# Kernel optimization log

Measured on AMD Instinct MI355X. Metric: run time of the kernel, lower is better.

## Reference

```python
import jax, jax.numpy as jnp
import numpy as np

RHO = 0.1

def setup_inputs() -> dict:
    key = jax.random.key(0)
    k1, k2 = jax.random.split(key)
    B, C, H, W = 64, 256, 56, 56
    features = jax.random.normal(k1, (B, C, H, W), dtype=jnp.float32)
    grad = jax.random.normal(k2, (B, C, H, W), dtype=jnp.float32)
    return {"features": features, "grad": grad}


def reference(features, grad):
    # attribution = relu(grad * features), elementwise
    attribution = jax.nn.relu(grad * features)
    B = attribution.shape[0]
    flat_attr = attribution.reshape(B, -1)          # [B, C*H*W]
    k = int(RHO * flat_attr.shape[1])               # static: 80281
    topk_val, _ = jax.lax.top_k(flat_attr, k)       # [B, k], descending
    threshold = topk_val[:, -1].reshape(-1, 1, 1, 1)  # k-th largest per sample
    mask = (attribution <= threshold).astype(features.dtype)
    return features * mask
```

## Files before the change

### kernel.cpp

```cpp
#include <hip/hip_runtime.h>

namespace {
constexpr int NS   = 64;
constexpr int NPS  = 802816;
constexpr int NPSV = NPS / 4;
constexpr unsigned KSEL = 80281u;
constexpr unsigned SENT = 0xFFFFFFFFu;
constexpr int NB   = 8192;
constexpr int GX   = 32;
constexpr int SEGV = NPSV / GX;
constexpr int SEG  = NPS / GX;
constexpr int PAIRCAP = 1024;
constexpr int CAP_LDS = 20480;
constexpr int BRB  = 8;
constexpr int CHUNKS = 128;
constexpr int CH_STRIDE = NPSV / CHUNKS;
constexpr unsigned RU_RANK = 12129u;
constexpr unsigned RL_RANK = 14086u;
constexpr int GXA  = 64;
constexpr int SEGCAP2 = 20736;
constexpr int TAILF4  = 1056;
typedef float f32x4 __attribute__((ext_vector_type(4)));
}

__device__ __forceinline__ void nt_store4(float4* dst, const float4& v) {
    f32x4 w; w.x = v.x; w.y = v.y; w.z = v.z; w.w = v.w;
    __builtin_nontemporal_store(w, reinterpret_cast<f32x4*>(dst));
}

template <int NBINS>
__device__ void select_in_lds(const unsigned* __restrict__ h, unsigned K,
                              unsigned* bin, unsigned* rem) {
    constexpr int BPT = NBINS / 256;
    __shared__ unsigned cs[256];
    __shared__ unsigned fB, fR;
    const int t = threadIdx.x;
    unsigned s = 0;
    for (int j = 0; j < BPT; ++j) s += h[t * BPT + j];
    cs[t] = s;
    if (t == 0) { fB = SENT; fR = 0u; }
    __syncthreads();
    unsigned suf = 0;
    for (int j = t + 1; j < 256; ++j) suf += cs[j];
    if (suf < K && suf + s >= K) {
        unsigned cur = suf;
        for (int j = BPT - 1; j >= 0; --j) {
            const unsigned c = h[t * BPT + j];
            if (cur < K && cur + c >= K) { fB = (unsigned)(t * BPT + j); fR = K - cur; break; }
            cur += c;
        }
    }
    __syncthreads();
    const unsigned rb = fB, rr = fR;
    __syncthreads();
    *bin = rb; *rem = rr;
}

__global__ __launch_bounds__(256) void bracket_kernel(const float4* __restrict__ f,
                                                      const float4* __restrict__ g,
                                                      unsigned short* __restrict__ bh,
                                                      unsigned* __restrict__ fail) {
    __shared__ unsigned h[NB];
    const int jb = blockIdx.x, b = blockIdx.y, t = threadIdx.x;
    if (jb == 0 && b == 0 && t == 0) fail[0] = 0u;
    for (int k = t; k < NB; k += 256) h[k] = 0u;
    __syncthreads();
    const size_t base = (size_t)b * NPSV;
#define HBIN(p) { if ((p) > 0.0f) atomicAdd(&h[__float_as_uint(p) >> 18], 1u); }
    for (int c = 0; c < CHUNKS / BRB; c += 2) {
        const int ch = jb * (CHUNKS / BRB) + c;
        const size_t i0 = base + (size_t)ch * CH_STRIDE + t;
        const size_t i1 = base + (size_t)(ch + 1) * CH_STRIDE + t;
        const float4 fa = f[i0], fb = f[i1];
        const float4 ga = g[i0], gb = g[i1];
        HBIN(fa.x * ga.x) HBIN(fa.y * ga.y) HBIN(fa.z * ga.z) HBIN(fa.w * ga.w)
        HBIN(fb.x * gb.x) HBIN(fb.y * gb.y) HBIN(fb.z * gb.z) HBIN(fb.w * gb.w)
    }
#undef HBIN
    __syncthreads();
    unsigned short* o = bh + (size_t)(b * BRB + jb) * NB;
    for (int k = t; k < NB; k += 256) o[k] = (unsigned short)h[k];
}

__global__ __launch_bounds__(256) void bracket_scan_kernel(const unsigned short* __restrict__ bh,
                                                           unsigned* __restrict__ binLU) {
    __shared__ unsigned h[NB];
    const int b = blockIdx.x, t = threadIdx.x;
    for (int k = t; k < NB; k += 256) {
        unsigned s = 0;
        const unsigned short* p = bh + (size_t)b * BRB * NB + k;
        for (int j = 0; j < BRB; ++j) s += p[(size_t)j * NB];
        h[k] = s;
    }
    __syncthreads();
    unsigned bU, rU, bL, rL;
    select_in_lds<NB>(h, RU_RANK, &bU, &rU);
    select_in_lds<NB>(h, RL_RANK, &bL, &rL);
    if (t == 0) {
        binLU[2 * b]     = (bL == SENT) ? 0u : bL;
        binLU[2 * b + 1] = (bU == SENT) ? (unsigned)(NB - 1) : bU;
    }
}

__global__ __launch_bounds__(256) void scatter0_kernel(const float4* __restrict__ f,
                                                       const float4* __restrict__ g,
                                                       float4* __restrict__ out,
                                                       unsigned* __restrict__ pv,
                                                       unsigned* __restrict__ ppos,
                                                       const unsigned* __restrict__ binLU,
                                                       unsigned* __restrict__ cnts,
                                                       unsigned* __restrict__ chis,
                                                       unsigned* __restrict__ fail) {
    const int j = blockIdx.x, b = blockIdx.y, t = threadIdx.x;
    const unsigned binL = binLU[2 * b], binU = binLU[2 * b + 1];
    __shared__ unsigned cnt;
    __shared__ unsigned wsum[4];
    if (t == 0) cnt = 0u;
    __syncthreads();
    const size_t segp = (size_t)(b * GX + j) * PAIRCAP;
    const size_t base = (size_t)b * NPSV + (size_t)j * SEGV;
    unsigned chi = 0;
#define PROC(FC, PC, I4, CIDX, OC) { \
        const float p_ = (FC) * (PC); \
        const unsigned u_ = __float_as_uint(p_); \
        const unsigned pre_ = u_ >> 18; \
        const bool pos_ = p_ > 0.0f; \
        const bool drop_ = pos_ && (pre_ > binU); \
        OC = drop_ ? 0.0f : (FC); \
        chi += drop_; \
        if (pos_ && pre_ >= binL && pre_ <= binU) { \
            const unsigned x_ = atomicAdd(&cnt, 1u); \
            if (x_ < PAIRCAP) { pv[segp + x_] = u_; ppos[segp + x_] = (unsigned)((j * SEGV + (I4)) * 4) + CIDX; } \
        } }
#define PROC4(FV, GV, I4, OV) \
        PROC(FV.x, GV.x, I4, 0u, OV.x) PROC(FV.y, GV.y, I4, 1u, OV.y) \
        PROC(FV.z, GV.z, I4, 2u, OV.z) PROC(FV.w, GV.w, I4, 3u, OV.w)

    constexpr int FULL = SEGV / 1024;
    for (int it = 0; it < FULL; ++it) {
        const int i0 = it * 1024 + t;
        const float4 f0 = f[base + i0];
        const float4 f1 = f[base + i0 + 256];
        const float4 f2 = f[base + i0 + 512];
        const float4 f3 = f[base + i0 + 768];
        const float4 g0 = g[base + i0];
        const float4 g1 = g[base + i0 + 256];
        const float4 g2 = g[base + i0 + 512];
        const float4 g3 = g[base + i0 + 768];
        float4 o0, o1, o2, o3;
        PROC4(f0, g0, i0,       o0)
        PROC4(f1, g1, i0 + 256, o1)
        PROC4(f2, g2, i0 + 512, o2)
        PROC4(f3, g3, i0 + 768, o3)
        nt_store4(&out[base + i0],       o0);
        nt_store4(&out[base + i0 + 256], o1);
        nt_store4(&out[base + i0 + 512], o2);
        nt_store4(&out[base + i0 + 768], o3);
    }
    {
        const int i = FULL * 1024 + t;
        if (i < SEGV) {
            const float4 fv = f[base + i];
            const float4 gv = g[base + i];
            float4 o;
            PROC4(fv, gv, i, o)
            nt_store4(&out[base + i], o);
        }
    }
#undef PROC4
#undef PROC
    for (int off = 32; off; off >>= 1) chi += __shfl_down(chi, off);
    if ((t & 63) == 0) wsum[t >> 6] = chi;
    __syncthreads();
    if (t == 0) {
        chis[b * GX + j] = wsum[0] + wsum[1] + wsum[2] + wsum[3];
        const unsigned c = cnt;
        cnts[b * GX + j] = c;
        if (c > PAIRCAP) fail[0] = 1u;
    }
}

__global__ __launch_bounds__(256) void select0_kernel(const unsigned* __restrict__ pv,
                                                      const unsigned* __restrict__ binLU,
                                                      const unsigned* __restrict__ cnts,
                                                      const unsigned* __restrict__ chis,
                                                      unsigned* __restrict__ fail,
                                                      float* __restrict__ thrF) {
    if (fail[0]) return;
    const int b = blockIdx.x, t = threadIdx.x;
    __shared__ unsigned vals[CAP_LDS];
    __shared__ unsigned hist[NB];
    __shared__ unsigned soff[GX + 1];
    __shared__ unsigned sh_chi;
    if (t == 0) {
        unsigned o = 0;
        for (int j = 0; j < GX; ++j) { soff[j] = o; o += cnts[b * GX + j]; }
        soff[GX] = o;
        unsigned c = 0;
        for (int j = 0; j < GX; ++j) c += chis[b * GX + j];
        sh_chi = c;
    }
    __syncthreads();
    const unsigned ncand = soff[GX];
    const unsigned chi = sh_chi;
    if (chi >= KSEL) { if (t == 0) fail[0] = 1u; return; }
    const unsigned Krem = KSEL - chi;
    if (Krem > ncand) {
        if (binLU[2 * b] == 0u) { if (t == 0) thrF[b] = 0.0f; }
        else                    { if (t == 0) fail[0] = 1u; }
        return;
    }
    if (ncand > CAP_LDS) { if (t == 0) fail[0] = 1u; return; }
    for (int j = 0; j < GX; ++j) {
        const unsigned c = soff[j + 1] - soff[j];
        const unsigned* s = pv + (size_t)(b * GX + j) * PAIRCAP;
        for (unsigned i = t; i < c; i += 256) vals[soff[j] + i] = s[i];
    }
    for (int k = t; k < NB; k += 256) hist[k] = 0u;
    __syncthreads();
    for (unsigned i = t; i < ncand; i += 256) atomicAdd(&hist[vals[i] >> 18], 1u);
    __syncthreads();
    unsigned P1, r1; select_in_lds<NB>(hist, Krem, &P1, &r1);
    __syncthreads();
    for (int k = t; k < NB; k += 256) hist[k] = 0u;
    __syncthreads();
    for (unsigned i = t; i < ncand; i += 256) {
        const unsigned u = vals[i];
        if ((u >> 18) == P1) atomicAdd(&hist[(u >> 5) & (NB - 1u)], 1u);
    }
    __syncthreads();
    unsigned P2, r2; select_in_lds<NB>(hist, r1, &P2, &r2);
    __syncthreads();
    if (t < 32) hist[t] = 0u;
    __syncthreads();
    const unsigned pref = (P1 << 13) | P2;
    for (unsigned i = t; i < ncand; i += 256) {
        const unsigned u = vals[i];
        if ((u >> 5) == pref) atomicAdd(&hist[u & 31u], 1u);
    }
    __syncthreads();
    if (t == 0) {
        unsigned cur = 0, b3 = 0;
        for (int q = 31; q >= 0; --q) {
            const unsigned c = hist[q];
            if (cur < r2 && cur + c >= r2) { b3 = (unsigned)q; break; }
            cur += c;
        }
        thrF[b] = __uint_as_float((P1 << 18) | (P2 << 5) | b3);
    }
}

__global__ __launch_bounds__(256) void fixup0_kernel(const unsigned* __restrict__ pv,
                                                     const unsigned* __restrict__ ppos,
                                                     const unsigned* __restrict__ cnts,
                                                     const unsigned* __restrict__ fail,
                                                     const float* __restrict__ thrF,
                                                     float* __restrict__ out) {
    if (fail[0]) return;
    const int j = blockIdx.x, b = blockIdx.y, t = threadIdx.x;
    const float thr = thrF[b];
    const unsigned c = cnts[b * GX + j];
    const unsigned* v = pv + (size_t)(b * GX + j) * PAIRCAP;
    const unsigned* q = ppos + (size_t)(b * GX + j) * PAIRCAP;
    float* o = out + (size_t)b * NPS;
    for (unsigned i = t; i < c; i += 256) {
        if (__uint_as_float(v[i]) > thr) o[q[i]] = 0.0f;
    }
}

__global__ __launch_bounds__(256) void scatter_fb_kernel(const float4* __restrict__ f,
                                                         const float4* __restrict__ g,
                                                         unsigned* __restrict__ list,
                                                         unsigned* __restrict__ cnts,
                                                         unsigned* __restrict__ chis,
                                                         const unsigned* __restrict__ fail,
                                                         int mode, int segCap) {
    if (mode == 1 && fail[0] == 0u) return;
    const int j = blockIdx.x, b = blockIdx.y, t = threadIdx.x;
    __shared__ unsigned cnt;
    if (t == 0) cnt = 0u;
    __syncthreads();
    unsigned* __restrict__ seg = list + (size_t)b * NPS + (size_t)j * SEG;
    const size_t base = (size_t)b * NPSV + (size_t)j * SEGV;
    for (int i = t; i < SEGV; i += 256) {
        const float4 fv = f[base + i];
        const float4 gv = g[base + i];
        const float p0 = fv.x * gv.x, p1 = fv.y * gv.y, p2 = fv.z * gv.z, p3 = fv.w * gv.w;
#define PROCF(p) { if ((p) > 0.0f) { const unsigned x = atomicAdd(&cnt, 1u); \
                   if ((int)x < segCap) seg[x] = __float_as_uint(p); } }
        PROCF(p0) PROCF(p1) PROCF(p2) PROCF(p3)
#undef PROCF
    }
    __syncthreads();
    if (t == 0) {
        cnts[b * GX + j] = (cnt > (unsigned)segCap) ? (unsigned)segCap : cnt;
        chis[b * GX + j] = 0u;
    }
}

__global__ __launch_bounds__(256) void select_fb_kernel(const unsigned* __restrict__ list,
                                                        const unsigned* __restrict__ cnts,
                                                        unsigned* __restrict__ fail,
                                                        float* __restrict__ thrF,
                                                        int mode) {
    if (mode == 1 && fail[0] == 0u) return;
    const int b = blockIdx.x, t = threadIdx.x;
    __shared__ unsigned h[NB];
    __shared__ unsigned segc[GX];
    if (t < GX) segc[t] = cnts[b * GX + t];
    __syncthreads();
    unsigned ncand = 0;
    for (int j = 0; j < GX; ++j) ncand += segc[j];
    if (KSEL > ncand) {
        if (t == 0) thrF[b] = 0.0f;
        return;
    }
    const unsigned* __restrict__ seg0 = list + (size_t)b * NPS;
    for (int k = t; k < NB; k += 256) h[k] = 0u;
    __syncthreads();
    for (int j = 0; j < GX; ++j) {
        const unsigned c = segc[j];
        const unsigned* s = seg0 + (size_t)j * SEG;
        for (unsigned i = t; i < c; i += 256) atomicAdd(&h[s[i] >> 18], 1u);
    }
    __syncthreads();
    unsigned P1, r1; select_in_lds<NB>(h, KSEL, &P1, &r1);
    __syncthreads();
    for (int k = t; k < NB; k += 256) h[k] = 0u;
    __syncthreads();
    for (int j = 0; j < GX; ++j) {
        const unsigned c = segc[j];
        const unsigned* s = seg0 + (size_t)j * SEG;
        for (unsigned i = t; i < c; i += 256) {
            const unsigned u = s[i];
            if ((u >> 18) == P1) atomicAdd(&h[(u >> 5) & (NB - 1u)], 1u);
        }
    }
    __syncthreads();
    unsigned P2, r2; select_in_lds<NB>(h, r1, &P2, &r2);
    __syncthreads();
    if (t < 32) h[t] = 0u;
    __syncthreads();
    const unsigned pref = (P1 << 13) | P2;
    for (int j = 0; j < GX; ++j) {
        const unsigned c = segc[j];
        const unsigned* s = seg0 + (size_t)j * SEG;
        for (unsigned i = t; i < c; i += 256) {
            const unsigned u = s[i];
            if ((u >> 5) == pref) atomicAdd(&h[u & 31u], 1u);
        }
    }
    __syncthreads();
    if (t == 0) {
        unsigned cur = 0, b3 = 0;
        for (int q = 31; q >= 0; --q) {
            const unsigned c = h[q];
            if (cur < r2 && cur + c >= r2) { b3 = (unsigned)q; break; }
            cur += c;
        }
        thrF[b] = __uint_as_float((P1 << 18) | (P2 << 5) | b3);
    }
}

__global__ __launch_bounds__(256) void apply_fb_kernel(const float4* __restrict__ f,
                                                       const float4* __restrict__ g,
                                                       const float* __restrict__ thrF,
                                                       float4* __restrict__ out,
                                                       const unsigned* __restrict__ fail,
                                                       int mode, int tailCut) {
    if (mode == 1 && fail[0] == 0u) return;
    const int b = blockIdx.y;
    const float thr = thrF[b];
    const size_t base = (size_t)b * NPSV;
    const int limit = NPSV - ((b == NS - 1) ? tailCut : 0);
    const int stride = gridDim.x * blockDim.x;
    for (int i = blockIdx.x * 256 + threadIdx.x; i < limit; i += stride) {
        const float4 fv = f[base + i];
        const float4 gv = g[base + i];
        float4 o;
        o.x = (fv.x * gv.x > thr) ? 0.0f : fv.x;
        o.y = (fv.y * gv.y > thr) ? 0.0f : fv.y;
        o.z = (fv.z * gv.z > thr) ? 0.0f : fv.z;
        o.w = (fv.w * gv.w > thr) ? 0.0f : fv.w;
        out[base + i] = o;
    }
}

__global__ void apply_tail_kernel(const float4* __restrict__ f, const float4* __restrict__ g,
                                  const float* __restrict__ thrF,
                                  float4* __restrict__ out, int tailCut) {
    const float thr = thrF[NS - 1];
    asm volatile("" :: "v"(thr));
    __syncthreads();
    const size_t base = (size_t)NS * NPSV - tailCut;
    for (int i = threadIdx.x; i < tailCut; i += 256) {
        const float4 fv = f[base + i];
        const float4 gv = g[base + i];
        float4 o;
        o.x = (fv.x * gv.x > thr) ? 0.0f : fv.x;
        o.y = (fv.y * gv.y > thr) ? 0.0f : fv.y;
        o.z = (fv.z * gv.z > thr) ? 0.0f : fv.z;
        o.w = (fv.w * gv.w > thr) ? 0.0f : fv.w;
        out[base + i] = o;
    }
}

extern "C" void kernel_launch(void* const* d_in, const int* in_sizes, int n_in,
                              void* d_out, int out_size, void* d_ws, size_t ws_size,
                              hipStream_t stream) {
    const float* f = (const float*)d_in[0];
    const float* g = (const float*)d_in[1];
    float* out = (float*)d_out;

    const size_t pairU32  = (size_t)NS * GX * PAIRCAP;
    const size_t brBytes  = (size_t)NS * BRB * NB * sizeof(unsigned short);
    const size_t bigBytes = (pairU32 * 8 > brBytes) ? pairU32 * 8 : brBytes;
    const size_t smallU32 = 2 * NS + NS * GX + NS * GX + 1 + NS;
    const size_t need     = bigBytes + smallU32 * 4;

    if (ws_size >= need) {
        char* w = (char*)d_ws;
        unsigned short* bh = (unsigned short*)w;
        unsigned* pv   = (unsigned*)w;
        unsigned* ppos = pv + pairU32;
        unsigned* sm   = (unsigned*)(w + bigBytes);
        unsigned* binLU = sm;
        unsigned* cnts  = binLU + 2 * NS;
        unsigned* chis  = cnts + NS * GX;
        unsigned* fail  = chis + NS * GX;
        float*    thrF  = (float*)(fail + 1);

        bracket_kernel<<<dim3(BRB, NS), 256, 0, stream>>>((const float4*)f, (const float4*)g,
                                                          bh, fail);
        bracket_scan_kernel<<<NS, 256, 0, stream>>>(bh, binLU);
        scatter0_kernel<<<dim3(GX, NS), 256, 0, stream>>>((const float4*)f, (const float4*)g,
                                                          (float4*)out, pv, ppos, binLU,
                                                          cnts, chis, fail);
        select0_kernel<<<NS, 256, 0, stream>>>(pv, binLU, cnts, chis, fail, thrF);
        fixup0_kernel<<<dim3(GX, NS), 256, 0, stream>>>(pv, ppos, cnts, fail, thrF, out);
        scatter_fb_kernel<<<dim3(GX, NS), 256, 0, stream>>>((const float4*)f, (const float4*)g,
                                                            (unsigned*)out, cnts, chis, fail,
                                                            1, SEG);
        select_fb_kernel<<<NS, 256, 0, stream>>>((const unsigned*)out, cnts, fail, thrF, 1);
        apply_fb_kernel<<<dim3(GXA, NS), 256, 0, stream>>>((const float4*)f, (const float4*)g,
                                                           thrF, (float4*)out, fail, 1, 0);
    } else {
        unsigned* list = (unsigned*)out;
        unsigned* sm   = (unsigned*)out + ((size_t)NS * NPS - 4 * TAILF4);
        unsigned* cnts = sm;
        unsigned* chis = cnts + NS * GX;
        unsigned* fail = chis + NS * GX;
        float*    thrF = (float*)(fail + 1);

        scatter_fb_kernel<<<dim3(GX, NS), 256, 0, stream>>>((const float4*)f, (const float4*)g,
                                                            list, cnts, chis, fail, 2, SEGCAP2);
        select_fb_kernel<<<NS, 256, 0, stream>>>(list, cnts, fail, thrF, 2);
        apply_fb_kernel<<<dim3(GXA, NS), 256, 0, stream>>>((const float4*)f, (const float4*)g,
                                                           thrF, (float4*)out, fail, 2, TAILF4);
        apply_tail_kernel<<<1, 256, 0, stream>>>((const float4*)f, (const float4*)g,
                                                 thrF, (float4*)out, TAILF4);
    }
}
```

Before: 218.9 us.

## Stage scatter candidates in LDS, software-prefetch loop, fuse fixup into select kernel

The scatter kernel now buffers candidate values and positions in shared memory and writes them to global memory in one coalesced pass at the end, instead of scattered per-atomic global writes. Its main loop changes from four independent float4 loads per iteration to a one-ahead register prefetch. The separate fixup kernel is folded into the select kernel, which zeroes above-threshold outputs directly from the LDS copy of the values, removing one launch and a reread. In exchange, the per-sample fixup now runs in only 64 blocks, and the prefetch loop keeps fewer loads in flight.

After: 230.0 us. 5.0% more time.

```diff
diff --git a/kernel.cpp b/kernel.cpp
--- a/kernel.cpp
+++ b/kernel.cpp
@@ -115,13 +115,14 @@
     const unsigned binL = binLU[2 * b], binU = binLU[2 * b + 1];
     __shared__ unsigned cnt;
     __shared__ unsigned wsum[4];
+    __shared__ unsigned lv[PAIRCAP];
+    __shared__ unsigned lp[PAIRCAP];
     if (t == 0) cnt = 0u;
     __syncthreads();
-    const size_t segp = (size_t)(b * GX + j) * PAIRCAP;
     const size_t base = (size_t)b * NPSV + (size_t)j * SEGV;
     unsigned chi = 0;
-#define PROC(FC, PC, I4, CIDX, OC) { \
-        const float p_ = (FC) * (PC); \
+#define PROC(FC, GC, IDX, CIDX, OC) { \
+        const float p_ = (FC) * (GC); \
         const unsigned u_ = __float_as_uint(p_); \
         const unsigned pre_ = u_ >> 18; \
         const bool pos_ = p_ > 0.0f; \
@@ -130,68 +131,61 @@
         chi += drop_; \
         if (pos_ && pre_ >= binL && pre_ <= binU) { \
             const unsigned x_ = atomicAdd(&cnt, 1u); \
-            if (x_ < PAIRCAP) { pv[segp + x_] = u_; ppos[segp + x_] = (unsigned)((j * SEGV + (I4)) * 4) + CIDX; } \
+            if (x_ < PAIRCAP) { lv[x_] = u_; lp[x_] = (unsigned)((IDX) * 4) + CIDX; } \
         } }
-#define PROC4(FV, GV, I4, OV) \
-        PROC(FV.x, GV.x, I4, 0u, OV.x) PROC(FV.y, GV.y, I4, 1u, OV.y) \
-        PROC(FV.z, GV.z, I4, 2u, OV.z) PROC(FV.w, GV.w, I4, 3u, OV.w)
-
-    constexpr int FULL = SEGV / 1024;
-    for (int it = 0; it < FULL; ++it) {
-        const int i0 = it * 1024 + t;
-        const float4 f0 = f[base + i0];
-        const float4 f1 = f[base + i0 + 256];
-        const float4 f2 = f[base + i0 + 512];
-        const float4 f3 = f[base + i0 + 768];
-        const float4 g0 = g[base + i0];
-        const float4 g1 = g[base + i0 + 256];
-        const float4 g2 = g[base + i0 + 512];
-        const float4 g3 = g[base + i0 + 768];
-        float4 o0, o1, o2, o3;
-        PROC4(f0, g0, i0,       o0)
-        PROC4(f1, g1, i0 + 256, o1)
-        PROC4(f2, g2, i0 + 512, o2)
-        PROC4(f3, g3, i0 + 768, o3)
-        nt_store4(&out[base + i0],       o0);
-        nt_store4(&out[base + i0 + 256], o1);
-        nt_store4(&out[base + i0 + 512], o2);
-        nt_store4(&out[base + i0 + 768], o3);
-    }
-    {
-        const int i = FULL * 1024 + t;
-        if (i < SEGV) {
-            const float4 fv = f[base + i];
-            const float4 gv = g[base + i];
-            float4 o;
-            PROC4(fv, gv, i, o)
-            nt_store4(&out[base + i], o);
-        }
+#define PROC4(FV, GV, IDX, OV) \
+        PROC(FV.x, GV.x, IDX, 0u, OV.x) PROC(FV.y, GV.y, IDX, 1u, OV.y) \
+        PROC(FV.z, GV.z, IDX, 2u, OV.z) PROC(FV.w, GV.w, IDX, 3u, OV.w)
+
+    constexpr int ITERS = SEGV / 256;
+    constexpr int TAIL0 = ITERS * 256;
+    float4 cf = f[base + t], cg = g[base + t];
+    for (int it = 0; it < ITERS; ++it) {
+        const int i = it * 256 + t;
+        float4 nf, ng;
+        if (it < ITERS - 1) { nf = f[base + i + 256]; ng = g[base + i + 256]; }
+        else if (t < SEGV - TAIL0) { nf = f[base + TAIL0 + t]; ng = g[base + TAIL0 + t]; }
+        float4 o;
+        PROC4(cf, cg, j * SEGV + i, o)
+        nt_store4(&out[base + i], o);
+        cf = nf; cg = ng;
+    }
+    if (t < SEGV - TAIL0) {
+        float4 o;
+        PROC4(cf, cg, j * SEGV + TAIL0 + t, o)
+        nt_store4(&out[base + TAIL0 + t], o);
     }
 #undef PROC4
 #undef PROC
     for (int off = 32; off; off >>= 1) chi += __shfl_down(chi, off);
     if ((t & 63) == 0) wsum[t >> 6] = chi;
     __syncthreads();
+    const unsigned ctot = cnt;
+    const unsigned c = (ctot > PAIRCAP) ? PAIRCAP : ctot;
+    const size_t segp = (size_t)(b * GX + j) * PAIRCAP;
+    for (unsigned k = t; k < c; k += 256) { pv[segp + k] = lv[k]; ppos[segp + k] = lp[k]; }
     if (t == 0) {
         chis[b * GX + j] = wsum[0] + wsum[1] + wsum[2] + wsum[3];
-        const unsigned c = cnt;
         cnts[b * GX + j] = c;
-        if (c > PAIRCAP) fail[0] = 1u;
+        if (ctot > PAIRCAP) fail[0] = 1u;
     }
 }
 
 __global__ __launch_bounds__(256) void select0_kernel(const unsigned* __restrict__ pv,
+                                                      const unsigned* __restrict__ ppos,
                                                       const unsigned* __restrict__ binLU,
                                                       const unsigned* __restrict__ cnts,
                                                       const unsigned* __restrict__ chis,
                                                       unsigned* __restrict__ fail,
-                                                      float* __restrict__ thrF) {
+                                                      float* __restrict__ thrF,
+                                                      float* __restrict__ out) {
     if (fail[0]) return;
     const int b = blockIdx.x, t = threadIdx.x;
     __shared__ unsigned vals[CAP_LDS];
     __shared__ unsigned hist[NB];
     __shared__ unsigned soff[GX + 1];
     __shared__ unsigned sh_chi;
+    __shared__ float sh_thr;
     if (t == 0) {
         unsigned o = 0;
         for (int j = 0; j < GX; ++j) { soff[j] = o; o += cnts[b * GX + j]; }
@@ -204,67 +198,66 @@
     const unsigned ncand = soff[GX];
     const unsigned chi = sh_chi;
     if (chi >= KSEL) { if (t == 0) fail[0] = 1u; return; }
+    if (ncand > CAP_LDS) { if (t == 0) fail[0] = 1u; return; }
     const unsigned Krem = KSEL - chi;
+    bool zeroThr = false;
     if (Krem > ncand) {
-        if (binLU[2 * b] == 0u) { if (t == 0) thrF[b] = 0.0f; }
-        else                    { if (t == 0) fail[0] = 1u; }
-        return;
-    }
-    if (ncand > CAP_LDS) { if (t == 0) fail[0] = 1u; return; }
+        if (binLU[2 * b] == 0u) zeroThr = true;
+        else { if (t == 0) fail[0] = 1u; return; }
+    }
     for (int j = 0; j < GX; ++j) {
         const unsigned c = soff[j + 1] - soff[j];
         const unsigned* s = pv + (size_t)(b * GX + j) * PAIRCAP;
         for (unsigned i = t; i < c; i += 256) vals[soff[j] + i] = s[i];
     }
-    for (int k = t; k < NB; k += 256) hist[k] = 0u;
-    __syncthreads();
-    for (unsigned i = t; i < ncand; i += 256) atomicAdd(&hist[vals[i] >> 18], 1u);
-    __syncthreads();
-    unsigned P1, r1; select_in_lds<NB>(hist, Krem, &P1, &r1);
-    __syncthreads();
-    for (int k = t; k < NB; k += 256) hist[k] = 0u;
-    __syncthreads();
-    for (unsigned i = t; i < ncand; i += 256) {
-        const unsigned u = vals[i];
-        if ((u >> 18) == P1) atomicAdd(&hist[(u >> 5) & (NB - 1u)], 1u);
-    }
-    __syncthreads();
-    unsigned P2, r2; select_in_lds<NB>(hist, r1, &P2, &r2);
-    __syncthreads();
-    if (t < 32) hist[t] = 0u;
-    __syncthreads();
-    const unsigned pref = (P1 << 13) | P2;
-    for (unsigned i = t; i < ncand; i += 256) {
-        const unsigned u = vals[i];
-        if ((u >> 5) == pref) atomicAdd(&hist[u & 31u], 1u);
-    }
-    __syncthreads();
-    if (t == 0) {
-        unsigned cur = 0, b3 = 0;
-        for (int q = 31; q >= 0; --q) {
-            const unsigned c = hist[q];
-            if (cur < r2 && cur + c >= r2) { b3 = (unsigned)q; break; }
-            cur += c;
-        }
-        thrF[b] = __uint_as_float((P1 << 18) | (P2 << 5) | b3);
-    }
-}
-
-__global__ __launch_bounds__(256) void fixup0_kernel(const unsigned* __restrict__ pv,
-                                                     const unsigned* __restrict__ ppos,
-                                                     const unsigned* __restrict__ cnts,
-                                                     const unsigned* __restrict__ fail,
-                                                     const float* __restrict__ thrF,
-                                                     float* __restrict__ out) {
-    if (fail[0]) return;
-    const int j = blockIdx.x, b = blockIdx.y, t = threadIdx.x;
-    const float thr = thrF[b];
-    const unsigned c = cnts[b * GX + j];
-    const unsigned* v = pv + (size_t)(b * GX + j) * PAIRCAP;
-    const unsigned* q = ppos + (size_t)(b * GX + j) * PAIRCAP;
-    float* o = out + (size_t)b * NPS;
-    for (unsigned i = t; i < c; i += 256) {
-        if (__uint_as_float(v[i]) > thr) o[q[i]] = 0.0f;
+    if (zeroThr) {
+        if (t == 0) { sh_thr = 0.0f; thrF[b] = 0.0f; }
+        __syncthreads();
+    } else {
+        for (int k = t; k < NB; k += 256) hist[k] = 0u;
+        __syncthreads();
+        for (unsigned i = t; i < ncand; i += 256) atomicAdd(&hist[vals[i] >> 18], 1u);
+        __syncthreads();
+        unsigned P1, r1; select_in_lds<NB>(hist, Krem, &P1, &r1);
+        __syncthreads();
+        for (int k = t; k < NB; k += 256) hist[k] = 0u;
+        __syncthreads();
+        for (unsigned i = t; i < ncand; i += 256) {
+            const unsigned u = vals[i];
+            if ((u >> 18) == P1) atomicAdd(&hist[(u >> 5) & (NB - 1u)], 1u);
+        }
+        __syncthreads();
+        unsigned P2, r2; select_in_lds<NB>(hist, r1, &P2, &r2);
+        __syncthreads();
+        if (t < 32) hist[t] = 0u;
+        __syncthreads();
+        const unsigned pref = (P1 << 13) | P2;
+        for (unsigned i = t; i < ncand; i += 256) {
+            const unsigned u = vals[i];
+            if ((u >> 5) == pref) atomicAdd(&hist[u & 31u], 1u);
+        }
+        __syncthreads();
+        if (t == 0) {
+            unsigned cur = 0, b3 = 0;
+            for (int q = 31; q >= 0; --q) {
+                const unsigned c = hist[q];
+                if (cur < r2 && cur + c >= r2) { b3 = (unsigned)q; break; }
+                cur += c;
+            }
+            const float thr = __uint_as_float((P1 << 18) | (P2 << 5) | b3);
+            sh_thr = thr; thrF[b] = thr;
+        }
+        __syncthreads();
+    }
+    const float thr = sh_thr;
+    float* ob = out + (size_t)b * NPS;
+    for (int j = 0; j < GX; ++j) {
+        const unsigned c = soff[j + 1] - soff[j];
+        const unsigned* qp = ppos + (size_t)(b * GX + j) * PAIRCAP;
+        const unsigned so = soff[j];
+        for (unsigned i = t; i < c; i += 256) {
+            if (__uint_as_float(vals[so + i]) > thr) ob[qp[i]] = 0.0f;
+        }
     }
 }
 
@@ -436,8 +429,7 @@
         scatter0_kernel<<<dim3(GX, NS), 256, 0, stream>>>((const float4*)f, (const float4*)g,
                                                           (float4*)out, pv, ppos, binLU,
                                                           cnts, chis, fail);
-        select0_kernel<<<NS, 256, 0, stream>>>(pv, binLU, cnts, chis, fail, thrF);
-        fixup0_kernel<<<dim3(GX, NS), 256, 0, stream>>>(pv, ppos, cnts, fail, thrF, out);
+        select0_kernel<<<NS, 256, 0, stream>>>(pv, ppos, binLU, cnts, chis, fail, thrF, out);
         scatter_fb_kernel<<<dim3(GX, NS), 256, 0, stream>>>((const float4*)f, (const float4*)g,
                                                             (unsigned*)out, cnts, chis, fail,
                                                             1, SEG);
```
